# Performance work log

Measured on AMD Instinct MI355X. Metric: run time of the kernel, lower is better.

Reference implementation:

```python
import jax, jax.numpy as jnp
import numpy as np

H, Hk, Hv, Dk, Dv, K = 1536, 8, 16, 64, 64, 4
KEY_DIM = Hk * Dk            # 512
VALUE_DIM = Hv * Dv          # 1024
CONV_DIM = 2 * KEY_DIM + VALUE_DIM  # 2048


def setup_inputs() -> dict:
    key = jax.random.key(0)
    ks = jax.random.split(key, 12)
    s = 0.02
    return {
        "hidden_states": jax.random.normal(ks[0], (1, H, 1, 1), jnp.float32),
        "W_qkv": jax.random.normal(ks[1], (CONV_DIM, H), jnp.float32) * s,
        "W_z": jax.random.normal(ks[2], (VALUE_DIM, H), jnp.float32) * s,
        "W_a": jax.random.normal(ks[3], (Hv, H), jnp.float32) * s,
        "W_b": jax.random.normal(ks[4], (Hv, H), jnp.float32) * s,
        "W_out": jax.random.normal(ks[5], (H, VALUE_DIM), jnp.float32) * s,
        "conv1d_weight": jax.random.normal(ks[6], (CONV_DIM, K), jnp.float32) * 0.1,
        "A_log": jax.random.normal(ks[7], (Hv,), jnp.float32) * 0.1,
        "dt_bias": jax.random.normal(ks[8], (Hv,), jnp.float32) * 0.1,
        "norm_weight": jnp.ones((Dv,), jnp.float32),
        "state": jax.random.normal(ks[9], (1, Hv, Dk, Dv), jnp.float32) * 0.05,
        "conv_cache": jax.random.normal(ks[10], (1, CONV_DIM, K - 1), jnp.float32) * 0.1,
    }


def _l2n(t):
    # l2_normalize with eps=1e-12 (matches torch rsqrt(sum(x^2)+eps))
    return t * jax.lax.rsqrt(jnp.sum(t * t, axis=-1, keepdims=True) + 1e-12)


def reference(hidden_states, W_qkv, W_z, W_a, W_b, W_out, conv1d_weight,
              A_log, dt_bias, norm_weight, state, conv_cache):
    x = hidden_states.reshape(-1)                       # [H]
    qkv = W_qkv @ x                                     # [CONV_DIM]
    z = (W_z @ x).reshape(Hv, Dv)                       # gate, [Hv, Dv]
    a = W_a @ x                                         # [Hv]
    beta = jax.nn.sigmoid(W_b @ x)                      # [Hv]

    # causal conv as weighted sum over cache + current token
    combined = jnp.concatenate([conv_cache[0], qkv[:, None]], axis=1)  # [CONV_DIM, K]
    conv_out = jax.nn.silu(jnp.sum(combined * conv1d_weight, axis=1))  # [CONV_DIM]

    q = conv_out[:KEY_DIM].reshape(Hk, Dk)
    k = conv_out[KEY_DIM:2 * KEY_DIM].reshape(Hk, Dk)
    v = conv_out[2 * KEY_DIM:].reshape(Hv, Dv)

    rep = Hv // Hk                                      # kv_group = 2
    q = jnp.repeat(q, rep, axis=0)                      # [Hv, Dk]
    k = jnp.repeat(k, rep, axis=0)
    q = _l2n(q) * (Dk ** -0.5)
    k = _l2n(k)

    # gated decay
    g = -jnp.exp(A_log) * jax.nn.softplus(a + dt_bias)  # [Hv]
    st = state[0] * jnp.exp(g)[:, None, None]           # [Hv, Dk, Dv]

    # delta-rule update
    retrieved = jnp.einsum('hkv,hk->hv', st, k)         # [Hv, Dv]
    delta = (v - retrieved) * beta[:, None]             # [Hv, Dv]
    new_state = st + jnp.einsum('hk,hv->hkv', k, delta) # [Hv, Dk, Dv]

    out = jnp.einsum('hkv,hk->hv', new_state, q)        # [Hv, Dv]

    # gated RMSNorm over Dv
    var = jnp.mean(out * out, axis=-1, keepdims=True)
    out = norm_weight * (out * jax.lax.rsqrt(var + 1e-6)) * jax.nn.silu(z)

    y = W_out @ out.reshape(-1)                         # [H]
    return y.reshape(1, -1, 1, 1)
```

## Files before the change

kernel.cpp:

```cpp
#include <hip/hip_runtime.h>

#define H 1536
#define HK 8
#define HV 16
#define DK 64
#define DV 64
#define KEY_DIM 512
#define VALUE_DIM 1024
#define CONV_DIM 2048
#define NROWS1 (CONV_DIM + VALUE_DIM + HV + HV)

__device__ __forceinline__ float wave_reduce_sum(float v) {
#pragma unroll
    for (int off = 32; off > 0; off >>= 1) v += __shfl_xor(v, off, 64);
    return v;
}

__global__ __launch_bounds__(256) void gemv_in(
        const float* __restrict__ x,
        const float* __restrict__ Wqkv, const float* __restrict__ Wz,
        const float* __restrict__ Wa,   const float* __restrict__ Wb,
        float* __restrict__ ws) {
    const int wave = threadIdx.x >> 6;
    const int lane = threadIdx.x & 63;
    const int row  = blockIdx.x * 4 + wave;
    const float* wrow;
    if (row < CONV_DIM)                      wrow = Wqkv + (size_t)row * H;
    else if (row < CONV_DIM + VALUE_DIM)     wrow = Wz + (size_t)(row - CONV_DIM) * H;
    else if (row < CONV_DIM + VALUE_DIM + HV)wrow = Wa + (size_t)(row - CONV_DIM - VALUE_DIM) * H;
    else                                     wrow = Wb + (size_t)(row - CONV_DIM - VALUE_DIM - HV) * H;
    const float4* w4 = (const float4*)wrow;
    const float4* x4 = (const float4*)x;
    float acc = 0.f;
#pragma unroll
    for (int j = 0; j < 6; ++j) {
        float4 a = w4[lane + 64 * j];
        float4 b = x4[lane + 64 * j];
        acc += a.x * b.x + a.y * b.y + a.z * b.z + a.w * b.w;
    }
    acc = wave_reduce_sum(acc);
    if (lane == 0) ws[row] = acc;
}

__global__ __launch_bounds__(256) void decode_core(
        const float* __restrict__ ws,
        const float* __restrict__ conv_w,
        const float* __restrict__ conv_cache,
        const float* __restrict__ A_log, const float* __restrict__ dt_bias,
        const float* __restrict__ norm_w,
        const float* __restrict__ state,
        float* __restrict__ out_gated) {
    const int h    = blockIdx.x;
    const int tid  = threadIdx.x;
    const int lane = tid & 63;
    const int grp  = tid >> 6;

    __shared__ float q_s[64], k_s[64], v_s[64];
    __shared__ float red_r[256], red_o[256];
    __shared__ float scal[3];

    if (grp < 3) {
        int i;
        if (grp == 0)      i = (h >> 1) * 64 + lane;
        else if (grp == 1) i = KEY_DIM + (h >> 1) * 64 + lane;
        else               i = 2 * KEY_DIM + h * 64 + lane;
        float raw = conv_cache[i * 3 + 0] * conv_w[i * 4 + 0]
                  + conv_cache[i * 3 + 1] * conv_w[i * 4 + 1]
                  + conv_cache[i * 3 + 2] * conv_w[i * 4 + 2]
                  + ws[i]                 * conv_w[i * 4 + 3];
        float c = raw / (1.f + expf(-raw));
        if (grp == 2) {
            v_s[lane] = c;
        } else {
            float ss  = wave_reduce_sum(c * c);
            float inv = rsqrtf(ss + 1e-12f);
            if (grp == 0) q_s[lane] = c * inv * 0.125f;
            else          k_s[lane] = c * inv;
        }
    } else if (lane == 0) {
        float aa = ws[CONV_DIM + VALUE_DIM + h] + dt_bias[h];
        float sp = (aa > 20.f) ? aa : log1pf(expf(aa));
        scal[0] = expf(-expf(A_log[h]) * sp);
        float braw = ws[CONV_DIM + VALUE_DIM + HV + h];
        scal[1] = 1.f / (1.f + expf(-braw));
    }
    __syncthreads();

    const float* st = state + (size_t)h * DK * DV;
    float pr = 0.f, po = 0.f;
    const int k0 = grp * 16;
#pragma unroll
    for (int kk = 0; kk < 16; ++kk) {
        float s = st[(k0 + kk) * 64 + lane];
        pr += s * k_s[k0 + kk];
        po += s * q_s[k0 + kk];
    }
    red_r[tid] = pr;
    red_o[tid] = po;
    if (grp == 0) {
        float t = wave_reduce_sum(k_s[lane] * q_s[lane]);
        if (lane == 0) scal[2] = t;
    }
    __syncthreads();

    if (tid < 64) {
        const float decay = scal[0], beta = scal[1], kq = scal[2];
        float r = (red_r[tid] + red_r[64 + tid] + red_r[128 + tid] + red_r[192 + tid]) * decay;
        float o = (red_o[tid] + red_o[64 + tid] + red_o[128 + tid] + red_o[192 + tid]) * decay;
        float delta = (v_s[tid] - r) * beta;
        float outv  = o + delta * kq;
        float ss  = wave_reduce_sum(outv * outv);
        float inv = rsqrtf(ss * (1.f / 64.f) + 1e-6f);
        float zz  = ws[CONV_DIM + h * 64 + tid];
        float gate = zz / (1.f + expf(-zz));
        out_gated[h * 64 + tid] = norm_w[tid] * outv * inv * gate;
    }
}

__global__ __launch_bounds__(256) void gemv_out(
        const float* __restrict__ Wout, const float* __restrict__ og,
        float* __restrict__ y) {
    const int wave = threadIdx.x >> 6;
    const int lane = threadIdx.x & 63;
    const int row  = blockIdx.x * 4 + wave;
    const float4* w4 = (const float4*)(Wout + (size_t)row * VALUE_DIM);
    const float4* g4 = (const float4*)og;
    float acc = 0.f;
#pragma unroll
    for (int j = 0; j < 4; ++j) {
        float4 a = w4[lane + 64 * j];
        float4 b = g4[lane + 64 * j];
        acc += a.x * b.x + a.y * b.y + a.z * b.z + a.w * b.w;
    }
    acc = wave_reduce_sum(acc);
    if (lane == 0) y[row] = acc;
}

extern "C" void kernel_launch(void* const* d_in, const int* in_sizes, int n_in,
                              void* d_out, int out_size, void* d_ws, size_t ws_size,
                              hipStream_t stream) {
    const float* x     = (const float*)d_in[0];
    const float* Wqkv  = (const float*)d_in[1];
    const float* Wz    = (const float*)d_in[2];
    const float* Wa    = (const float*)d_in[3];
    const float* Wb    = (const float*)d_in[4];
    const float* Wout  = (const float*)d_in[5];
    const float* convw = (const float*)d_in[6];
    const float* Alog  = (const float*)d_in[7];
    const float* dtb   = (const float*)d_in[8];
    const float* normw = (const float*)d_in[9];
    const float* state = (const float*)d_in[10];
    const float* cch   = (const float*)d_in[11];

    float* ws = (float*)d_ws;
    float* og = ws + NROWS1;
    float* y  = (float*)d_out;

    gemv_in<<<NROWS1 / 4, 256, 0, stream>>>(x, Wqkv, Wz, Wa, Wb, ws);
    decode_core<<<HV, 256, 0, stream>>>(ws, convw, cch, Alog, dtb, normw, state, og);
    gemv_out<<<H / 4, 256, 0, stream>>>(Wout, og, y);
}
```

Before: 96.89 us.

## Fuse three decode kernels into one persistent kernel with grid barriers

Merges the input GEMV, the per-head delta-rule core and the output GEMV into a single 776-block kernel synchronised by two software grid barriers built on atomics. W_out rows are prefetched into registers before the first barrier, so that load overlaps the input GEMV and the core stage. The aim is to remove two kernel launch boundaries and their gaps. In exchange it depends on all 776 blocks being co-resident (4 blocks per CU), adds a memset launch and atomic spin costs, and leaves most blocks idle during the core stage.

New measurement: 256.3 us. 2.64x slower.

```diff
diff --git a/kernel.cpp b/kernel.cpp
--- a/kernel.cpp
+++ b/kernel.cpp
@@ -9,6 +9,7 @@
 #define VALUE_DIM 1024
 #define CONV_DIM 2048
 #define NROWS1 (CONV_DIM + VALUE_DIM + HV + HV)
+#define NBLK 776
 
 __device__ __forceinline__ float wave_reduce_sum(float v) {
 #pragma unroll
@@ -16,124 +17,146 @@
     return v;
 }
 
-__global__ __launch_bounds__(256) void gemv_in(
+__device__ __forceinline__ void grid_barrier(int* counter, int* gen) {
+    __syncthreads();
+    if (threadIdx.x == 0) {
+        int g = __hip_atomic_load(gen, __ATOMIC_RELAXED, __HIP_MEMORY_SCOPE_AGENT);
+        int old = __hip_atomic_fetch_add(counter, 1, __ATOMIC_ACQ_REL, __HIP_MEMORY_SCOPE_AGENT);
+        if (old == NBLK - 1) {
+            __hip_atomic_store(counter, 0, __ATOMIC_RELAXED, __HIP_MEMORY_SCOPE_AGENT);
+            __hip_atomic_store(gen, g + 1, __ATOMIC_RELEASE, __HIP_MEMORY_SCOPE_AGENT);
+        } else {
+            while (__hip_atomic_load(gen, __ATOMIC_ACQUIRE, __HIP_MEMORY_SCOPE_AGENT) == g)
+                __builtin_amdgcn_s_sleep(1);
+        }
+    }
+    __syncthreads();
+}
+
+__global__ __launch_bounds__(256, 4) void fused_decode(
         const float* __restrict__ x,
         const float* __restrict__ Wqkv, const float* __restrict__ Wz,
         const float* __restrict__ Wa,   const float* __restrict__ Wb,
-        float* __restrict__ ws) {
-    const int wave = threadIdx.x >> 6;
-    const int lane = threadIdx.x & 63;
-    const int row  = blockIdx.x * 4 + wave;
-    const float* wrow;
-    if (row < CONV_DIM)                      wrow = Wqkv + (size_t)row * H;
-    else if (row < CONV_DIM + VALUE_DIM)     wrow = Wz + (size_t)(row - CONV_DIM) * H;
-    else if (row < CONV_DIM + VALUE_DIM + HV)wrow = Wa + (size_t)(row - CONV_DIM - VALUE_DIM) * H;
-    else                                     wrow = Wb + (size_t)(row - CONV_DIM - VALUE_DIM - HV) * H;
-    const float4* w4 = (const float4*)wrow;
-    const float4* x4 = (const float4*)x;
-    float acc = 0.f;
-#pragma unroll
-    for (int j = 0; j < 6; ++j) {
-        float4 a = w4[lane + 64 * j];
-        float4 b = x4[lane + 64 * j];
-        acc += a.x * b.x + a.y * b.y + a.z * b.z + a.w * b.w;
-    }
-    acc = wave_reduce_sum(acc);
-    if (lane == 0) ws[row] = acc;
-}
-
-__global__ __launch_bounds__(256) void decode_core(
-        const float* __restrict__ ws,
-        const float* __restrict__ conv_w,
-        const float* __restrict__ conv_cache,
+        const float* __restrict__ Wout,
+        const float* __restrict__ conv_w, const float* __restrict__ conv_cache,
         const float* __restrict__ A_log, const float* __restrict__ dt_bias,
-        const float* __restrict__ norm_w,
-        const float* __restrict__ state,
-        float* __restrict__ out_gated) {
-    const int h    = blockIdx.x;
+        const float* __restrict__ norm_w, const float* __restrict__ state,
+        float* __restrict__ ws, float* __restrict__ og,
+        int* counter, int* gen,
+        float* __restrict__ y) {
+    const int blk  = blockIdx.x;
     const int tid  = threadIdx.x;
+    const int wave = tid >> 6;
     const int lane = tid & 63;
-    const int grp  = tid >> 6;
 
     __shared__ float q_s[64], k_s[64], v_s[64];
     __shared__ float red_r[256], red_o[256];
     __shared__ float scal[3];
 
-    if (grp < 3) {
-        int i;
-        if (grp == 0)      i = (h >> 1) * 64 + lane;
-        else if (grp == 1) i = KEY_DIM + (h >> 1) * 64 + lane;
-        else               i = 2 * KEY_DIM + h * 64 + lane;
-        float raw = conv_cache[i * 3 + 0] * conv_w[i * 4 + 0]
-                  + conv_cache[i * 3 + 1] * conv_w[i * 4 + 1]
-                  + conv_cache[i * 3 + 2] * conv_w[i * 4 + 2]
-                  + ws[i]                 * conv_w[i * 4 + 3];
-        float c = raw / (1.f + expf(-raw));
-        if (grp == 2) {
-            v_s[lane] = c;
-        } else {
-            float ss  = wave_reduce_sum(c * c);
-            float inv = rsqrtf(ss + 1e-12f);
-            if (grp == 0) q_s[lane] = c * inv * 0.125f;
-            else          k_s[lane] = c * inv;
+    float4 wreg[4];
+    const int orow = blk * 4 + wave;
+    if (blk < 384) {
+        const float4* w4 = (const float4*)(Wout + (size_t)orow * VALUE_DIM);
+#pragma unroll
+        for (int j = 0; j < 4; ++j) wreg[j] = w4[lane + 64 * j];
+    }
+
+    {
+        const int row = blk * 4 + wave;
+        const float* wrow;
+        if (row < CONV_DIM)                       wrow = Wqkv + (size_t)row * H;
+        else if (row < CONV_DIM + VALUE_DIM)      wrow = Wz + (size_t)(row - CONV_DIM) * H;
+        else if (row < CONV_DIM + VALUE_DIM + HV) wrow = Wa + (size_t)(row - CONV_DIM - VALUE_DIM) * H;
+        else                                      wrow = Wb + (size_t)(row - CONV_DIM - VALUE_DIM - HV) * H;
+        const float4* w4 = (const float4*)wrow;
+        const float4* x4 = (const float4*)x;
+        float acc = 0.f;
+#pragma unroll
+        for (int j = 0; j < 6; ++j) {
+            float4 a = w4[lane + 64 * j];
+            float4 b = x4[lane + 64 * j];
+            acc += a.x * b.x + a.y * b.y + a.z * b.z + a.w * b.w;
         }
-    } else if (lane == 0) {
-        float aa = ws[CONV_DIM + VALUE_DIM + h] + dt_bias[h];
-        float sp = (aa > 20.f) ? aa : log1pf(expf(aa));
-        scal[0] = expf(-expf(A_log[h]) * sp);
-        float braw = ws[CONV_DIM + VALUE_DIM + HV + h];
-        scal[1] = 1.f / (1.f + expf(-braw));
+        acc = wave_reduce_sum(acc);
+        if (lane == 0) ws[row] = acc;
     }
-    __syncthreads();
 
-    const float* st = state + (size_t)h * DK * DV;
-    float pr = 0.f, po = 0.f;
-    const int k0 = grp * 16;
+    grid_barrier(counter, gen);
+
+    if (blk < HV) {
+        const int h = blk;
+        const int grp = wave;
+        if (grp < 3) {
+            int i;
+            if (grp == 0)      i = (h >> 1) * 64 + lane;
+            else if (grp == 1) i = KEY_DIM + (h >> 1) * 64 + lane;
+            else               i = 2 * KEY_DIM + h * 64 + lane;
+            float raw = conv_cache[i * 3 + 0] * conv_w[i * 4 + 0]
+                      + conv_cache[i * 3 + 1] * conv_w[i * 4 + 1]
+                      + conv_cache[i * 3 + 2] * conv_w[i * 4 + 2]
+                      + ws[i]                 * conv_w[i * 4 + 3];
+            float c = raw / (1.f + expf(-raw));
+            if (grp == 2) {
+                v_s[lane] = c;
+            } else {
+                float ss  = wave_reduce_sum(c * c);
+                float inv = rsqrtf(ss + 1e-12f);
+                if (grp == 0) q_s[lane] = c * inv * 0.125f;
+                else          k_s[lane] = c * inv;
+            }
+        } else if (lane == 0) {
+            float aa = ws[CONV_DIM + VALUE_DIM + h] + dt_bias[h];
+            float sp = (aa > 20.f) ? aa : log1pf(expf(aa));
+            scal[0] = expf(-expf(A_log[h]) * sp);
+            float braw = ws[CONV_DIM + VALUE_DIM + HV + h];
+            scal[1] = 1.f / (1.f + expf(-braw));
+        }
+        __syncthreads();
+
+        const float* st = state + (size_t)h * DK * DV;
+        float pr = 0.f, po = 0.f;
+        const int k0 = grp * 16;
 #pragma unroll
-    for (int kk = 0; kk < 16; ++kk) {
-        float s = st[(k0 + kk) * 64 + lane];
-        pr += s * k_s[k0 + kk];
-        po += s * q_s[k0 + kk];
+        for (int kk = 0; kk < 16; ++kk) {
+            float s = st[(k0 + kk) * 64 + lane];
+            pr += s * k_s[k0 + kk];
+            po += s * q_s[k0 + kk];
+        }
+        red_r[tid] = pr;
+        red_o[tid] = po;
+        if (grp == 0) {
+            float t = wave_reduce_sum(k_s[lane] * q_s[lane]);
+            if (lane == 0) scal[2] = t;
+        }
+        __syncthreads();
+
+        if (tid < 64) {
+            const float decay = scal[0], beta = scal[1], kq = scal[2];
+            float r = (red_r[tid] + red_r[64 + tid] + red_r[128 + tid] + red_r[192 + tid]) * decay;
+            float o = (red_o[tid] + red_o[64 + tid] + red_o[128 + tid] + red_o[192 + tid]) * decay;
+            float delta = (v_s[tid] - r) * beta;
+            float outv  = o + delta * kq;
+            float ss  = wave_reduce_sum(outv * outv);
+            float inv = rsqrtf(ss * (1.f / 64.f) + 1e-6f);
+            float zz  = ws[CONV_DIM + h * 64 + tid];
+            float gate = zz / (1.f + expf(-zz));
+            og[h * 64 + tid] = norm_w[tid] * outv * inv * gate;
+        }
     }
-    red_r[tid] = pr;
-    red_o[tid] = po;
-    if (grp == 0) {
-        float t = wave_reduce_sum(k_s[lane] * q_s[lane]);
-        if (lane == 0) scal[2] = t;
+
+    grid_barrier(counter, gen);
+
+    if (blk < 384) {
+        const float4* g4 = (const float4*)og;
+        float acc = 0.f;
+#pragma unroll
+        for (int j = 0; j < 4; ++j) {
+            float4 b = g4[lane + 64 * j];
+            acc += wreg[j].x * b.x + wreg[j].y * b.y + wreg[j].z * b.z + wreg[j].w * b.w;
+        }
+        acc = wave_reduce_sum(acc);
+        if (lane == 0) y[orow] = acc;
     }
-    __syncthreads();
-
-    if (tid < 64) {
-        const float decay = scal[0], beta = scal[1], kq = scal[2];
-        float r = (red_r[tid] + red_r[64 + tid] + red_r[128 + tid] + red_r[192 + tid]) * decay;
-        float o = (red_o[tid] + red_o[64 + tid] + red_o[128 + tid] + red_o[192 + tid]) * decay;
-        float delta = (v_s[tid] - r) * beta;
-        float outv  = o + delta * kq;
-        float ss  = wave_reduce_sum(outv * outv);
-        float inv = rsqrtf(ss * (1.f / 64.f) + 1e-6f);
-        float zz  = ws[CONV_DIM + h * 64 + tid];
-        float gate = zz / (1.f + expf(-zz));
-        out_gated[h * 64 + tid] = norm_w[tid] * outv * inv * gate;
-    }
-}
-
-__global__ __launch_bounds__(256) void gemv_out(
-        const float* __restrict__ Wout, const float* __restrict__ og,
-        float* __restrict__ y) {
-    const int wave = threadIdx.x >> 6;
-    const int lane = threadIdx.x & 63;
-    const int row  = blockIdx.x * 4 + wave;
-    const float4* w4 = (const float4*)(Wout + (size_t)row * VALUE_DIM);
-    const float4* g4 = (const float4*)og;
-    float acc = 0.f;
-#pragma unroll
-    for (int j = 0; j < 4; ++j) {
-        float4 a = w4[lane + 64 * j];
-        float4 b = g4[lane + 64 * j];
-        acc += a.x * b.x + a.y * b.y + a.z * b.z + a.w * b.w;
-    }
-    acc = wave_reduce_sum(acc);
-    if (lane == 0) y[row] = acc;
 }
 
 extern "C" void kernel_launch(void* const* d_in, const int* in_sizes, int n_in,
@@ -154,9 +177,12 @@
 
     float* ws = (float*)d_ws;
     float* og = ws + NROWS1;
-    float* y  = (float*)d_out;
+    int* barrier_mem = (int*)((char*)d_ws + (size_t)(NROWS1 + VALUE_DIM) * 4);
+    float* y = (float*)d_out;
 
-    gemv_in<<<NROWS1 / 4, 256, 0, stream>>>(x, Wqkv, Wz, Wa, Wb, ws);
-    decode_core<<<HV, 256, 0, stream>>>(ws, convw, cch, Alog, dtb, normw, state, og);
-    gemv_out<<<H / 4, 256, 0, stream>>>(Wout, og, y);
+    hipMemsetAsync(barrier_mem, 0, 2 * sizeof(int), stream);
+
+    fused_decode<<<NBLK, 256, 0, stream>>>(
+        x, Wqkv, Wz, Wa, Wb, Wout, convw, cch, Alog, dtb, normw, state,
+        ws, og, barrier_mem, barrier_mem + 1, y);
 }
```
